# Kernel tuning notes

Hardware: AMD Instinct MI355X
Metric: run time of the kernel (lower is better)

## Reference

```python
import jax, jax.numpy as jnp
import numpy as np

NUM_HEADS = 12
THETA = 10000.0


def _rope(x, pos):
    # x: [B, H, S, dk]; interleaved even/odd pair rotation
    dk = x.shape[-1]
    freqs = THETA ** (-jnp.arange(dk // 2, dtype=jnp.float32) * 2.0 / dk)  # [dk/2]
    ang = pos.astype(jnp.float32)[:, None] * freqs                         # [S, dk/2]
    cos, sin = jnp.cos(ang), jnp.sin(ang)
    x1, x2 = x[..., 0::2], x[..., 1::2]
    rot = jnp.stack([x1 * cos - x2 * sin, x1 * sin + x2 * cos], axis=-1)
    return rot.reshape(x.shape)


def setup_inputs() -> dict:
    key = jax.random.key(0)
    ks = jax.random.split(key, 5)
    B, S, D = 4, 2048, 768
    w_scale = 1.0 / np.sqrt(D).astype(np.float32)
    x = jax.random.normal(ks[0], (B, S, D), dtype=jnp.float32)
    Wq = jax.random.normal(ks[1], (D, D), dtype=jnp.float32) * w_scale
    Wk = jax.random.normal(ks[2], (D, D), dtype=jnp.float32) * w_scale
    Wv = jax.random.normal(ks[3], (D, D), dtype=jnp.float32) * w_scale
    Wo = jax.random.normal(ks[4], (D, D), dtype=jnp.float32) * w_scale
    token_positions = jnp.arange(S, dtype=jnp.int32)
    return {"x": x, "Wq": Wq, "Wk": Wk, "Wv": Wv, "Wo": Wo,
            "token_positions": token_positions}


def reference(x, Wq, Wk, Wv, Wo, token_positions):
    B, S, D = x.shape
    H = NUM_HEADS
    dk = D // H
    # bias-free linear layers: y = x @ W^T (torch Linear weight convention)
    q = (x @ Wq.T).reshape(B, S, H, dk).transpose(0, 2, 1, 3)  # [B,H,S,dk]
    k = (x @ Wk.T).reshape(B, S, H, dk).transpose(0, 2, 1, 3)
    v = (x @ Wv.T).reshape(B, S, H, dk).transpose(0, 2, 1, 3)
    q = _rope(q, token_positions)
    k = _rope(k, token_positions)
    scores = jnp.einsum('bhqd,bhkd->bhqk', q, k) / np.float32(np.sqrt(dk))
    causal = jnp.tril(jnp.ones((S, S), dtype=bool))
    scores = jnp.where(causal, scores, -jnp.inf)
    attn = jax.nn.softmax(scores, axis=-1)                      # [B,H,S,S]
    out = jnp.einsum('bhqk,bhkd->bhqd', attn, v)
    out = out.transpose(0, 2, 1, 3).reshape(B, S, D)
    return out @ Wo.T
```

## Files before the change

### kernel.cpp

```cpp
#include <hip/hip_runtime.h>
#include <cstdint>
#include <cstddef>

#define NTOK 8192
#define SLEN 2048
#define DM   768
#define NH   12
#define DKH  64

typedef __attribute__((ext_vector_type(8))) short bf16x8;
typedef __attribute__((ext_vector_type(4))) float f32x4;

__device__ __forceinline__ float b2f(unsigned short u) {
  return __uint_as_float(((unsigned)u) << 16);
}
__device__ __forceinline__ unsigned short f2b(float f) {
  unsigned u = __float_as_uint(f);
  u += 0x7fffu + ((u >> 16) & 1u);
  return (unsigned short)(u >> 16);
}
__device__ __forceinline__ unsigned cvtpk(float lo, float hi) {
  unsigned r;
  asm("v_cvt_pk_bf16_f32 %0, %1, %2" : "=v"(r) : "v"(lo), "v"(hi));
  return r;
}

__device__ __forceinline__ void gld16(const void* g, void* l) {
  __builtin_amdgcn_global_load_lds(
      (const __attribute__((address_space(1))) void*)g,
      (__attribute__((address_space(3))) void*)l, 16, 0, 0);
}

#define BAR_DRAIN() do {                                  \
    asm volatile("s_waitcnt vmcnt(0)" ::: "memory");      \
    __builtin_amdgcn_s_barrier();                         \
    __builtin_amdgcn_sched_barrier(0);                    \
  } while (0)
#define BAR_KEEP4() do {                                  \
    asm volatile("s_waitcnt vmcnt(4)" ::: "memory");      \
    __builtin_amdgcn_s_barrier();                         \
    __builtin_amdgcn_sched_barrier(0);                    \
  } while (0)

__global__ void cast_all_kernel(const float* __restrict__ x,
                                const float* __restrict__ w0,
                                const float* __restrict__ w1,
                                const float* __restrict__ w2,
                                const float* __restrict__ w3,
                                unsigned short* __restrict__ xb,
                                unsigned short* __restrict__ wb) {
  const int bid = blockIdx.x, tid = threadIdx.x;
  const float* src;
  unsigned short* dst;
  size_t i;
  if (bid < 3072) {
    src = x; dst = xb; i = (size_t)bid * 256 + tid;
  } else {
    const int wbid = bid - 3072;
    const int w = wbid / 288;
    src = (w == 0) ? w0 : (w == 1) ? w1 : (w == 2) ? w2 : w3;
    dst = wb + (size_t)w * DM * DM;
    i = (size_t)(wbid - w * 288) * 256 + tid;
  }
  const float4* p = (const float4*)(src + i * 8);
  float4 a = p[0], b = p[1];
  union { unsigned short h[8]; bf16x8 v; } u;
  u.h[0] = f2b(a.x); u.h[1] = f2b(a.y); u.h[2] = f2b(a.z); u.h[3] = f2b(a.w);
  u.h[4] = f2b(b.x); u.h[5] = f2b(b.y); u.h[6] = f2b(b.z); u.h[7] = f2b(b.w);
  *(bf16x8*)(dst + i * 8) = u.v;
}

__global__ __launch_bounds__(256, 3) void gemm_qkv_kernel(
    const unsigned short* __restrict__ A, const unsigned short* __restrict__ Ball,
    unsigned short* __restrict__ Qb, unsigned short* __restrict__ Kb,
    unsigned short* __restrict__ VTout,
    const int* __restrict__ pos) {
  const int K = DM;
  const int tid = threadIdx.x, wid = tid >> 6, lane = tid & 63;
  const int lrow = lane & 15, g = lane >> 4, lk8 = g * 8;
  const int m0 = blockIdx.y * 64, n0 = blockIdx.x * 128;
  const int wm = (wid >> 1) * 32, wn = (wid & 1) * 64;
  const int sr = wid * 8 + (lane >> 3), sc = (lane & 7) * 8;
  const int ssw = sc ^ ((sr & 7) << 3);
  __shared__ unsigned short At[64 * 64];
  __shared__ unsigned short Bt[128 * 64];
  f32x4 acc[2][4] = {};

  const unsigned short* ap = A    + (size_t)(m0 + sr) * K + ssw;
  const unsigned short* bp = Ball + (size_t)(n0 + sr) * K + ssw;

  int aoff[2][2], boff[2][4];
#pragma unroll
  for (int ks = 0; ks < 2; ++ks) {
#pragma unroll
    for (int mi = 0; mi < 2; ++mi) {
      int ra = wm + mi * 16 + lrow;
      aoff[ks][mi] = (ra * 64 + ((ks * 32 + lk8) ^ ((ra & 7) << 3))) * 2;
    }
#pragma unroll
    for (int ni = 0; ni < 4; ++ni) {
      int rb = wn + ni * 16 + lrow;
      boff[ks][ni] = (rb * 64 + ((ks * 32 + lk8) ^ ((rb & 7) << 3))) * 2;
    }
  }
  const char* Atc = (const char*)At;
  const char* Btc = (const char*)Bt;

  const int nk = K >> 6;
  for (int kk = 0; kk < nk; ++kk) {
    __syncthreads();
    gld16(ap,          &At[(wid * 8) * 64]);
    gld16(ap + 32 * K, &At[(32 + wid * 8) * 64]);
#pragma unroll
    for (int rnd = 0; rnd < 4; ++rnd)
      gld16(bp + rnd * 32 * K, &Bt[(rnd * 32 + wid * 8) * 64]);
    ap += 64; bp += 64;
    __syncthreads();
    bf16x8 af[2][2], bfr[2][4];
#pragma unroll
    for (int ks = 0; ks < 2; ++ks) {
#pragma unroll
      for (int mi = 0; mi < 2; ++mi)
        af[ks][mi] = *(const bf16x8*)(Atc + aoff[ks][mi]);
#pragma unroll
      for (int ni = 0; ni < 4; ++ni)
        bfr[ks][ni] = *(const bf16x8*)(Btc + boff[ks][ni]);
    }
#pragma unroll
    for (int ks = 0; ks < 2; ++ks)
#pragma unroll
      for (int mi = 0; mi < 2; ++mi)
#pragma unroll
        for (int ni = 0; ni < 4; ++ni)
          acc[mi][ni] = __builtin_amdgcn_mfma_f32_16x16x32_bf16(
              bfr[ks][ni], af[ks][mi], acc[mi][ni], 0, 0, 0);
  }

  const int nsec = blockIdx.x / 6;
  const int nn0 = n0 - nsec * 768;

  if (nsec == 2) {
#pragma unroll
    for (int mi = 0; mi < 2; ++mi) {
      const int m = m0 + wm + mi * 16 + lrow;
      const int bb = m >> 11, st = m & (SLEN - 1);
      const int scol = (st & ~63) | (st & 35) |
                       (((st >> 4) & 1) << 2) | (((st >> 2) & 1) << 3) |
                       (((st >> 3) & 1) << 4);
#pragma unroll
      for (int ni = 0; ni < 4; ++ni) {
        const int nb = nn0 + wn + ni * 16 + g * 4;
        const int hh = nb >> 6, dd = nb & 63;
        unsigned short* dst =
            VTout + ((size_t)(bb * NH + hh) * DKH + dd) * SLEN + scol;
#pragma unroll
        for (int r = 0; r < 4; ++r)
          dst[(size_t)r * SLEN] = f2b(acc[mi][ni][r]);
      }
    }
    return;
  }

  unsigned short* Cp = (nsec == 0) ? Qb : Kb;
  float frq[4][2];
#pragma unroll
  for (int ni = 0; ni < 4; ++ni)
#pragma unroll
    for (int rp = 0; rp < 2; ++rp)
      frq[ni][rp] = exp2f(
          (float)(((wn + ni * 16 + g * 4 + rp * 2) & 63) >> 1) *
          -0.4152410118609203f);
#pragma unroll
  for (int mi = 0; mi < 2; ++mi) {
    const int m = m0 + wm + mi * 16 + lrow;
    const float ps = (float)pos[m & (SLEN - 1)];
#pragma unroll
    for (int ni = 0; ni < 4; ++ni) {
#pragma unroll
      for (int rp = 0; rp < 2; ++rp) {
        float sn, cs;
        __sincosf(ps * frq[ni][rp], &sn, &cs);
        float x1 = acc[mi][ni][2 * rp], x2 = acc[mi][ni][2 * rp + 1];
        acc[mi][ni][2 * rp]     = fmaf(x1, cs, -x2 * sn);
        acc[mi][ni][2 * rp + 1] = fmaf(x1, sn, x2 * cs);
      }
      union { unsigned u[2]; ushort4 s; } o;
      o.u[0] = cvtpk(acc[mi][ni][0], acc[mi][ni][1]);
      o.u[1] = cvtpk(acc[mi][ni][2], acc[mi][ni][3]);
      *(ushort4*)&Cp[(size_t)m * DM + nn0 + wn + ni * 16 + g * 4] = o.s;
    }
  }
}

__global__ __launch_bounds__(256, 3) void gemm_out_kernel(
    const unsigned short* __restrict__ A, const unsigned short* __restrict__ B,
    float* __restrict__ C) {
  const int K = DM, N = DM;
  const int tid = threadIdx.x, wid = tid >> 6, lane = tid & 63;
  const int lrow = lane & 15, g = lane >> 4, lk8 = g * 8;
  const int m0 = blockIdx.y * 64, n0 = blockIdx.x * 128;
  const int wm = (wid >> 1) * 32, wn = (wid & 1) * 64;
  const int sr = wid * 8 + (lane >> 3), sc = (lane & 7) * 8;
  const int ssw = sc ^ ((sr & 7) << 3);
  __shared__ unsigned short At[64 * 64];
  __shared__ unsigned short Bt[128 * 64];
  f32x4 acc[2][4] = {};

  const unsigned short* ap = A + (size_t)(m0 + sr) * K + ssw;
  const unsigned short* bp = B + (size_t)(n0 + sr) * K + ssw;

  int aoff[2][2], boff[2][4];
#pragma unroll
  for (int ks = 0; ks < 2; ++ks) {
#pragma unroll
    for (int mi = 0; mi < 2; ++mi) {
      int ra = wm + mi * 16 + lrow;
      aoff[ks][mi] = (ra * 64 + ((ks * 32 + lk8) ^ ((ra & 7) << 3))) * 2;
    }
#pragma unroll
    for (int ni = 0; ni < 4; ++ni) {
      int rb = wn + ni * 16 + lrow;
      boff[ks][ni] = (rb * 64 + ((ks * 32 + lk8) ^ ((rb & 7) << 3))) * 2;
    }
  }
  const char* Atc = (const char*)At;
  const char* Btc = (const char*)Bt;

  const int nk = K >> 6;
  for (int kk = 0; kk < nk; ++kk) {
    __syncthreads();
    gld16(ap,          &At[(wid * 8) * 64]);
    gld16(ap + 32 * K, &At[(32 + wid * 8) * 64]);
#pragma unroll
    for (int rnd = 0; rnd < 4; ++rnd)
      gld16(bp + rnd * 32 * K, &Bt[(rnd * 32 + wid * 8) * 64]);
    ap += 64; bp += 64;
    __syncthreads();
    bf16x8 af[2][2], bfr[2][4];
#pragma unroll
    for (int ks = 0; ks < 2; ++ks) {
#pragma unroll
      for (int mi = 0; mi < 2; ++mi)
        af[ks][mi] = *(const bf16x8*)(Atc + aoff[ks][mi]);
#pragma unroll
      for (int ni = 0; ni < 4; ++ni)
        bfr[ks][ni] = *(const bf16x8*)(Btc + boff[ks][ni]);
    }
#pragma unroll
    for (int ks = 0; ks < 2; ++ks)
#pragma unroll
      for (int mi = 0; mi < 2; ++mi)
#pragma unroll
        for (int ni = 0; ni < 4; ++ni)
          acc[mi][ni] = __builtin_amdgcn_mfma_f32_16x16x32_bf16(
              bfr[ks][ni], af[ks][mi], acc[mi][ni], 0, 0, 0);
  }

#pragma unroll
  for (int mi = 0; mi < 2; ++mi) {
    const int m = m0 + wm + mi * 16 + lrow;
#pragma unroll
    for (int ni = 0; ni < 4; ++ni)
      *(f32x4*)&C[(size_t)m * N + n0 + wn + ni * 16 + g * 4] = acc[mi][ni];
  }
}

__global__ __launch_bounds__(256, 3) void attn_kernel(
    const unsigned short* __restrict__ Q, const unsigned short* __restrict__ Kg,
    const unsigned short* __restrict__ VT, unsigned short* __restrict__ O) {
  const int bh = blockIdx.x;
  const int y = blockIdx.y;
  const int qA = y, qB = 31 - y;
  const int ntA = qA + 1, ntB = qB + 1;
  const int b = bh / NH, h = bh - b * NH;
  const size_t base = ((size_t)b * SLEN) * DM + h * DKH;
  const size_t vbase = (size_t)bh * DKH * SLEN;
  const int tid = threadIdx.x, wid = tid >> 6, lane = tid & 63;
  const int lrow = lane & 15, g = lane >> 4;
  const int rloc = wid * 16 + lrow;

  __shared__ unsigned short Kt[3][64 * 64];
  __shared__ unsigned short Vt[3][64 * 64];

  bf16x8 qfA[2], qfB[2];
#pragma unroll
  for (int ks = 0; ks < 2; ++ks) {
    union { unsigned short h[8]; bf16x8 v; } u;
    u.v = *(const bf16x8*)&Q[base + (size_t)(qA * 64 + rloc) * DM + ks * 32 + g * 8];
#pragma unroll
    for (int j = 0; j < 8; ++j)
      u.h[j] = f2b(b2f(u.h[j]) * 0.18033688011112042f);
    qfA[ks] = u.v;
    u.v = *(const bf16x8*)&Q[base + (size_t)(qB * 64 + rloc) * DM + ks * 32 + g * 8];
#pragma unroll
    for (int j = 0; j < 8; ++j)
      u.h[j] = f2b(b2f(u.h[j]) * 0.18033688011112042f);
    qfB[ks] = u.v;
  }

  union { unsigned short h[8]; bf16x8 v; } one_u;
#pragma unroll
  for (int j = 0; j < 8; ++j) one_u.h[j] = 0x3F80;
  const bf16x8 ones = one_u.v;

  f32x4 oaccA[4] = {}, oaccB[4] = {};
  f32x4 lA = {}, lB = {};

  const int srow = wid * 8 + (lane >> 3);
  const int ssw = ((lane & 7) * 8) ^ ((srow & 7) << 3);
  const unsigned short* kp = Kg + base + (size_t)srow * DM + ssw;
  const unsigned short* vp = VT + vbase + (size_t)srow * SLEN + ssw;

  int roff[2][4];
#pragma unroll
  for (int ks = 0; ks < 2; ++ks)
#pragma unroll
    for (int ni = 0; ni < 4; ++ni) {
      int rr = ni * 16 + lrow;
      roff[ks][ni] = (rr * 64 + ((ks * 32 + g * 8) ^ ((rr & 7) << 3))) * 2;
    }

  auto stage = [&](int buf) {
    gld16(kp,             &Kt[buf][(wid * 8) * 64]);
    gld16(kp + 32 * DM,   &Kt[buf][(32 + wid * 8) * 64]);
    gld16(vp,             &Vt[buf][(wid * 8) * 64]);
    gld16(vp + 32 * SLEN, &Vt[buf][(32 + wid * 8) * 64]);
    kp += 64 * DM;
    vp += 64;
  };

  auto computeSub = [&](const bf16x8 (&qf)[2], f32x4 (&oacc)[4], f32x4& l_acc,
                        bool diag, int buf) {
    const char* Ksb = (const char*)&Kt[buf][0];
    const char* Vsb = (const char*)&Vt[buf][0];

    f32x4 sa[4] = {};
    __builtin_amdgcn_s_setprio(1);
#pragma unroll
    for (int ks = 0; ks < 2; ++ks)
#pragma unroll
      for (int ni = 0; ni < 4; ++ni) {
        bf16x8 kf = *(const bf16x8*)(Ksb + roff[ks][ni]);
        sa[ni] = __builtin_amdgcn_mfma_f32_16x16x32_bf16(
            kf, qf[ks], sa[ni], 0, 0, 0);
      }
    __builtin_amdgcn_s_setprio(0);

    if (diag) {
#pragma unroll
      for (int ni = 0; ni < 4; ++ni)
#pragma unroll
        for (int r = 0; r < 4; ++r)
          if (ni * 16 + g * 4 + r > rloc) sa[ni][r] = -1e30f;
    }

#pragma unroll
    for (int ni = 0; ni < 4; ++ni)
#pragma unroll
      for (int r = 0; r < 4; ++r)
        sa[ni][r] = exp2f(sa[ni][r]);

    bf16x8 pf[2];
#pragma unroll
    for (int ks = 0; ks < 2; ++ks) {
      union { unsigned u[4]; bf16x8 v; } uu;
      uu.u[0] = cvtpk(sa[2 * ks][0],     sa[2 * ks][1]);
      uu.u[1] = cvtpk(sa[2 * ks][2],     sa[2 * ks][3]);
      uu.u[2] = cvtpk(sa[2 * ks + 1][0], sa[2 * ks + 1][1]);
      uu.u[3] = cvtpk(sa[2 * ks + 1][2], sa[2 * ks + 1][3]);
      pf[ks] = uu.v;
    }

    __builtin_amdgcn_s_setprio(1);
#pragma unroll
    for (int ks = 0; ks < 2; ++ks) {
#pragma unroll
      for (int ni = 0; ni < 4; ++ni) {
        bf16x8 vf = *(const bf16x8*)(Vsb + roff[ks][ni]);
        oacc[ni] = __builtin_amdgcn_mfma_f32_16x16x32_bf16(
            vf, pf[ks], oacc[ni], 0, 0, 0);
      }
      l_acc = __builtin_amdgcn_mfma_f32_16x16x32_bf16(
          ones, pf[ks], l_acc, 0, 0, 0);
    }
    __builtin_amdgcn_s_setprio(0);
  };

  stage(0);
  int buf = 0, bufn = 1;
  for (int t = 0; t < ntB; ++t) {
    if (t + 1 < ntB) {
      stage(bufn);
      BAR_KEEP4();
    } else {
      BAR_DRAIN();
    }
    if (t < ntA) computeSub(qfA, oaccA, lA, t == qA, buf);
    computeSub(qfB, oaccB, lB, t == qB, buf);
    buf = bufn;
    bufn = (bufn == 2) ? 0 : bufn + 1;
  }

  {
    const float inv = 1.f / lA[0];
    const int qrow = qA * 64 + rloc;
#pragma unroll
    for (int ni = 0; ni < 4; ++ni) {
      union { unsigned u[2]; ushort4 s; } o;
      o.u[0] = cvtpk(oaccA[ni][0] * inv, oaccA[ni][1] * inv);
      o.u[1] = cvtpk(oaccA[ni][2] * inv, oaccA[ni][3] * inv);
      *(ushort4*)&O[base + (size_t)qrow * DM + ni * 16 + g * 4] = o.s;
    }
  }
  {
    const float inv = 1.f / lB[0];
    const int qrow = qB * 64 + rloc;
#pragma unroll
    for (int ni = 0; ni < 4; ++ni) {
      union { unsigned u[2]; ushort4 s; } o;
      o.u[0] = cvtpk(oaccB[ni][0] * inv, oaccB[ni][1] * inv);
      o.u[1] = cvtpk(oaccB[ni][2] * inv, oaccB[ni][3] * inv);
      *(ushort4*)&O[base + (size_t)qrow * DM + ni * 16 + g * 4] = o.s;
    }
  }
}

extern "C" void kernel_launch(void* const* d_in, const int* in_sizes, int n_in,
                              void* d_out, int out_size, void* d_ws, size_t ws_size,
                              hipStream_t stream) {
  const float* x  = (const float*)d_in[0];
  const float* Wq = (const float*)d_in[1];
  const float* Wk = (const float*)d_in[2];
  const float* Wv = (const float*)d_in[3];
  const float* Wo = (const float*)d_in[4];
  const int* pos  = (const int*)d_in[5];
  float* out = (float*)d_out;

  char* ws = (char*)d_ws;
  size_t off = 0;
  auto carve = [&](size_t bytes) -> void* {
    void* p = ws + off;
    off += (bytes + 255) & ~(size_t)255;
    return p;
  };
  unsigned short* xb  = (unsigned short*)carve((size_t)NTOK * DM * 2);
  unsigned short* wqb = (unsigned short*)carve((size_t)DM * DM * 2 * 4);
  unsigned short* wob = wqb + (size_t)3 * DM * DM;
  unsigned short* Qb  = (unsigned short*)carve((size_t)NTOK * DM * 2);
  unsigned short* Kb  = (unsigned short*)carve((size_t)NTOK * DM * 2);
  unsigned short* Ab  = (unsigned short*)carve((size_t)NTOK * DM * 2);
  unsigned short* VTb = (unsigned short*)carve((size_t)4 * NH * DKH * SLEN * 2);

  cast_all_kernel<<<dim3(3072 + 4 * 288), dim3(256), 0, stream>>>(
      x, Wq, Wk, Wv, Wo, xb, wqb);

  gemm_qkv_kernel<<<dim3(18, 128), dim3(256), 0, stream>>>(
      xb, wqb, Qb, Kb, VTb, pos);

  attn_kernel<<<dim3(48, 16), dim3(256), 0, stream>>>(Qb, Kb, VTb, Ab);

  gemm_out_kernel<<<dim3(6, 128), dim3(256), 0, stream>>>(Ab, wob, out);
}
```

Before: 118.7 us.

## Split paired causal q-tiles into one q-tile per attention block

The attention kernel previously had each block handle two query tiles (y and 31-y) so causal work per block was balanced. Now each block handles a single 64-row query tile, the grid doubles to 32 tiles per head, and launch bounds rise to 4 blocks per CU. The K/V stream drops from a triple buffer with a keep-4 wait to a double buffer that fully drains at each step. This aims for higher occupancy and less register pressure, but each K/V tile is now loaded once per query tile instead of being shared by two, block work becomes uneven, and the full drain exposes load latency.

```diff
diff --git a/kernel.cpp b/kernel.cpp
--- a/kernel.cpp
+++ b/kernel.cpp
@@ -33,11 +33,6 @@
 
 #define BAR_DRAIN() do {                                  \
     asm volatile("s_waitcnt vmcnt(0)" ::: "memory");      \
-    __builtin_amdgcn_s_barrier();                         \
-    __builtin_amdgcn_sched_barrier(0);                    \
-  } while (0)
-#define BAR_KEEP4() do {                                  \
-    asm volatile("s_waitcnt vmcnt(4)" ::: "memory");      \
     __builtin_amdgcn_s_barrier();                         \
     __builtin_amdgcn_sched_barrier(0);                    \
   } while (0)
@@ -265,13 +260,12 @@
   }
 }
 
-__global__ __launch_bounds__(256, 3) void attn_kernel(
+__global__ __launch_bounds__(256, 4) void attn_kernel(
     const unsigned short* __restrict__ Q, const unsigned short* __restrict__ Kg,
     const unsigned short* __restrict__ VT, unsigned short* __restrict__ O) {
   const int bh = blockIdx.x;
-  const int y = blockIdx.y;
-  const int qA = y, qB = 31 - y;
-  const int ntA = qA + 1, ntB = qB + 1;
+  const int s = 31 - (int)blockIdx.y;
+  const int nt = s + 1;
   const int b = bh / NH, h = bh - b * NH;
   const size_t base = ((size_t)b * SLEN) * DM + h * DKH;
   const size_t vbase = (size_t)bh * DKH * SLEN;
@@ -279,23 +273,18 @@
   const int lrow = lane & 15, g = lane >> 4;
   const int rloc = wid * 16 + lrow;
 
-  __shared__ unsigned short Kt[3][64 * 64];
-  __shared__ unsigned short Vt[3][64 * 64];
-
-  bf16x8 qfA[2], qfB[2];
+  __shared__ unsigned short Kt[2][64 * 64];
+  __shared__ unsigned short Vt[2][64 * 64];
+
+  bf16x8 qf[2];
 #pragma unroll
   for (int ks = 0; ks < 2; ++ks) {
     union { unsigned short h[8]; bf16x8 v; } u;
-    u.v = *(const bf16x8*)&Q[base + (size_t)(qA * 64 + rloc) * DM + ks * 32 + g * 8];
+    u.v = *(const bf16x8*)&Q[base + (size_t)(s * 64 + rloc) * DM + ks * 32 + g * 8];
 #pragma unroll
     for (int j = 0; j < 8; ++j)
       u.h[j] = f2b(b2f(u.h[j]) * 0.18033688011112042f);
-    qfA[ks] = u.v;
-    u.v = *(const bf16x8*)&Q[base + (size_t)(qB * 64 + rloc) * DM + ks * 32 + g * 8];
-#pragma unroll
-    for (int j = 0; j < 8; ++j)
-      u.h[j] = f2b(b2f(u.h[j]) * 0.18033688011112042f);
-    qfB[ks] = u.v;
+    qf[ks] = u.v;
   }
 
   union { unsigned short h[8]; bf16x8 v; } one_u;
@@ -303,8 +292,8 @@
   for (int j = 0; j < 8; ++j) one_u.h[j] = 0x3F80;
   const bf16x8 ones = one_u.v;
 
-  f32x4 oaccA[4] = {}, oaccB[4] = {};
-  f32x4 lA = {}, lB = {};
+  f32x4 oacc[4] = {};
+  f32x4 l_acc = {};
 
   const int srow = wid * 8 + (lane >> 3);
   const int ssw = ((lane & 7) * 8) ^ ((srow & 7) << 3);
@@ -329,8 +318,7 @@
     vp += 64;
   };
 
-  auto computeSub = [&](const bf16x8 (&qf)[2], f32x4 (&oacc)[4], f32x4& l_acc,
-                        bool diag, int buf) {
+  auto compute = [&](int t, int buf) {
     const char* Ksb = (const char*)&Kt[buf][0];
     const char* Vsb = (const char*)&Vt[buf][0];
 
@@ -346,7 +334,7 @@
       }
     __builtin_amdgcn_s_setprio(0);
 
-    if (diag) {
+    if (t == s) {
 #pragma unroll
       for (int ni = 0; ni < 4; ++ni)
 #pragma unroll
@@ -387,41 +375,23 @@
   };
 
   stage(0);
-  int buf = 0, bufn = 1;
-  for (int t = 0; t < ntB; ++t) {
-    if (t + 1 < ntB) {
-      stage(bufn);
-      BAR_KEEP4();
-    } else {
-      BAR_DRAIN();
-    }
-    if (t < ntA) computeSub(qfA, oaccA, lA, t == qA, buf);
-    computeSub(qfB, oaccB, lB, t == qB, buf);
-    buf = bufn;
-    bufn = (bufn == 2) ? 0 : bufn + 1;
-  }
-
-  {
-    const float inv = 1.f / lA[0];
-    const int qrow = qA * 64 + rloc;
-#pragma unroll
-    for (int ni = 0; ni < 4; ++ni) {
-      union { unsigned u[2]; ushort4 s; } o;
-      o.u[0] = cvtpk(oaccA[ni][0] * inv, oaccA[ni][1] * inv);
-      o.u[1] = cvtpk(oaccA[ni][2] * inv, oaccA[ni][3] * inv);
-      *(ushort4*)&O[base + (size_t)qrow * DM + ni * 16 + g * 4] = o.s;
-    }
-  }
-  {
-    const float inv = 1.f / lB[0];
-    const int qrow = qB * 64 + rloc;
-#pragma unroll
-    for (int ni = 0; ni < 4; ++ni) {
-      union { unsigned u[2]; ushort4 s; } o;
-      o.u[0] = cvtpk(oaccB[ni][0] * inv, oaccB[ni][1] * inv);
-      o.u[1] = cvtpk(oaccB[ni][2] * inv, oaccB[ni][3] * inv);
-      *(ushort4*)&O[base + (size_t)qrow * DM + ni * 16 + g * 4] = o.s;
-    }
+  BAR_DRAIN();
+  int cur = 0;
+  for (int t = 0; t < nt; ++t) {
+    if (t + 1 < nt) stage(cur ^ 1);
+    compute(t, cur);
+    BAR_DRAIN();
+    cur ^= 1;
+  }
+
+  const float inv = 1.f / l_acc[0];
+  const int qrow = s * 64 + rloc;
+#pragma unroll
+  for (int ni = 0; ni < 4; ++ni) {
+    union { unsigned u[2]; ushort4 s4; } o;
+    o.u[0] = cvtpk(oacc[ni][0] * inv, oacc[ni][1] * inv);
+    o.u[1] = cvtpk(oacc[ni][2] * inv, oacc[ni][3] * inv);
+    *(ushort4*)&O[base + (size_t)qrow * DM + ni * 16 + g * 4] = o.s4;
   }
 }
 
@@ -457,7 +427,7 @@
   gemm_qkv_kernel<<<dim3(18, 128), dim3(256), 0, stream>>>(
       xb, wqb, Qb, Kb, VTb, pos);
 
-  attn_kernel<<<dim3(48, 16), dim3(256), 0, stream>>>(Qb, Kb, VTb, Ab);
+  attn_kernel<<<dim3(48, 32), dim3(256), 0, stream>>>(Qb, Kb, VTb, Ab);
 
   gemm_out_kernel<<<dim3(6, 128), dim3(256), 0, stream>>>(Ab, wob, out);
 }
```

Result: no change. 117.1 us (median of 4 runs) (-1.4%).
